# Kernel tuning notes

Hardware: AMD Instinct MI355X
Metric: run time of the kernel (lower is better)

The kernel has to match this reference:

```python
import jax, jax.numpy as jnp
import numpy as np

V = 50257   # vocab_size
D = 128     # embed_dim
B = 1024    # batch of center words
C = 10      # context window size


def setup_inputs() -> dict:
    key = jax.random.key(0)
    ks = jax.random.split(key, 12)
    s = 0.05  # small init scale for linear weights
    return {
        "center_id": jax.random.randint(ks[0], (B,), 0, V),
        "context_ids": jax.random.randint(ks[1], (B, C), 0, V),
        "epsilon": jax.random.normal(ks[2], (D,), dtype=jnp.float32),
        # embedding tables init uniform(-1, 1) as in the torch module
        "emb": jax.random.uniform(ks[3], (V, D), minval=-1.0, maxval=1.0, dtype=jnp.float32),
        "prior_means": jax.random.uniform(ks[4], (V, D), minval=-1.0, maxval=1.0, dtype=jnp.float32),
        "prior_vars": jax.random.uniform(ks[5], (V, D), minval=-1.0, maxval=1.0, dtype=jnp.float32),
        "W_enc": jax.random.normal(ks[6], (2 * D, 2 * D), dtype=jnp.float32) * s,
        "b_enc": jnp.zeros((2 * D,), dtype=jnp.float32),
        "W_mean": jax.random.normal(ks[7], (2 * D, D), dtype=jnp.float32) * s,
        "b_mean": jnp.zeros((D,), dtype=jnp.float32),
        "W_var": jax.random.normal(ks[8], (2 * D, D), dtype=jnp.float32) * s,
        "b_var": jnp.zeros((D,), dtype=jnp.float32),
        "W_vocab": jax.random.normal(ks[9], (D, V), dtype=jnp.float32) * s,
        "b_vocab": jnp.zeros((V,), dtype=jnp.float32),
    }


def reference(center_id, context_ids, epsilon, emb, prior_means, prior_vars,
              W_enc, b_enc, W_mean, b_mean, W_var, b_var, W_vocab, b_vocab):
    ce = emb[center_id]                       # [B, D]
    cx = emb[context_ids]                     # [B, C, D]
    enc_in = jnp.concatenate(
        [jnp.broadcast_to(ce[:, None, :], cx.shape), cx], axis=-1)  # [B, C, 2D]
    h = jax.nn.relu(enc_in @ W_enc + b_enc).sum(axis=1)  # [B, 2D]
    mean = h @ W_mean + b_mean                           # [B, D]
    var = jax.nn.softplus(h @ W_var + b_var)             # [B, D] (diag cov s0)
    z = mean + jnp.exp(var / 2.0) * epsilon              # single shared epsilon [D]
    logits = z @ W_vocab + b_vocab                        # [B, V]
    logp = jax.nn.log_softmax(logits, axis=1)             # log(categorical)

    pm = prior_means[center_id]                           # m1 [B, D]
    pv = jax.nn.softplus(prior_vars[center_id])           # diag cov s1 [B, D]
    diff = pm - mean
    # closed-form diagonal Gaussian KL, identical math to the
    # trace/inverse/det formulation over diagflat matrices in the source
    kl = 0.5 * jnp.sum(var / pv + diff * diff / pv - 1.0
                       + jnp.log(pv) - jnp.log(var), axis=1)  # [B]

    # reconstruction: sum_k log categorical[i, context_ids[i, k]]
    rec = jnp.take_along_axis(logp, context_ids, axis=1).sum(axis=1)  # [B]

    return jnp.mean(rec - kl)
```

## Files before the change

### kernel.cpp

```cpp
#include <hip/hip_runtime.h>
#include <math.h>

#define VV 50257
#define VPAD 50304
#define DD 128
#define BB 1024
#define CC 10

typedef short bf16x8 __attribute__((ext_vector_type(8)));
typedef float f32x4 __attribute__((ext_vector_type(4)));

__device__ inline float bf2f(unsigned short u) {
    return __uint_as_float(((unsigned)u) << 16);
}
__device__ inline unsigned short f2bf(float f) {
    unsigned u = __float_as_uint(f);
    unsigned r = ((u >> 16) & 1) + 0x7FFF;
    return (unsigned short)((u + r) >> 16);
}


__global__ __launch_bounds__(256) void k_prep(
    const float* __restrict__ Wv, const float* __restrict__ W_enc,
    unsigned short* __restrict__ WvP, unsigned short* __restrict__ WeP)
{
    const int bid = blockIdx.x, tid = threadIdx.x;

    if (bid < 786) {
        __shared__ float tile[128][65];
        const int v0 = bid * 64;
#pragma unroll
        for (int i = 0; i < 32; ++i) {
            int idx = tid + i * 256;
            int k = idx >> 6, j = idx & 63;
            int v = v0 + j;
            tile[k][j] = (v < VV) ? Wv[(size_t)k * VV + v] : 0.f;
        }
        __syncthreads();
#pragma unroll
        for (int i = 0; i < 4; ++i) {
            int c = i * 256 + tid;
            int l15 = c & 15, q = (c >> 4) & 3, kI = (c >> 6) & 3, g = c >> 8;
            bf16x8 o;
#pragma unroll
            for (int e = 0; e < 8; ++e)
                o[e] = (short)f2bf(tile[kI * 32 + q * 8 + e][g * 16 + l15]);
            size_t vg = (size_t)bid * 4 + g;
            *(bf16x8*)(WvP + ((vg * 4 + kI) * 64 + q * 16 + l15) * 8) = o;
        }
        return;
    }

    __shared__ float tl[256][17];
    const int jg = bid - 786;
#pragma unroll
    for (int i = 0; i < 16; ++i) {
        int idx = i * 256 + tid;
        int k = idx >> 4, j = idx & 15;
        tl[k][j] = W_enc[(size_t)k * 256 + jg * 16 + j];
    }
    __syncthreads();
#pragma unroll
    for (int i = 0; i < 2; ++i) {
        int c = i * 256 + tid;
        int l15 = c & 15, q = (c >> 4) & 3, kI = c >> 6;
        bf16x8 o;
#pragma unroll
        for (int e = 0; e < 8; ++e)
            o[e] = (short)f2bf(tl[kI * 32 + q * 8 + e][l15]);
        *(bf16x8*)(WeP + (((size_t)jg * 8 + kI) * 64 + q * 16 + l15) * 8) = o;
    }
}

__global__ __launch_bounds__(256) void k_enc(
    const int* __restrict__ center_id, const int* __restrict__ context_ids,
    const float* __restrict__ emb, const unsigned short* __restrict__ WeP,
    const float* __restrict__ b_enc, unsigned short* __restrict__ enc_relu)
{
    __shared__ __align__(16) unsigned short As[64 * 256];
    __shared__ __align__(16) unsigned short Cs[64][136];
    const int tid  = threadIdx.x;
    const int lane = tid & 63;
    const int wid  = tid >> 6;
    const int wm   = wid & 1;
    const int wn   = wid >> 1;
    const int quad = lane >> 4;
    const int l15  = lane & 15;

    const int b0 = blockIdx.x * 64;
    const int c  = blockIdx.y;
    const int n0 = blockIdx.z * 128;

    const int rlane = tid >> 4;
    const int c8    = tid & 15;
    const int kIc   = c8 >> 2, qc = c8 & 3;
#pragma unroll
    for (int p = 0; p < 4; ++p) {
        int r = p * 16 + rlane;
        int rid_ce = center_id[b0 + r];
        int rid_cx = context_ids[(b0 + r) * CC + c];
        const float* s0 = emb + (size_t)rid_ce * 128 + c8 * 8;
        const float* s1 = emb + (size_t)rid_cx * 128 + c8 * 8;
        float4 a0 = *(const float4*)s0, a1 = *(const float4*)(s0 + 4);
        float4 b0v = *(const float4*)s1, b1v = *(const float4*)(s1 + 4);
        bf16x8 oa, ob;
        oa[0] = (short)f2bf(a0.x); oa[1] = (short)f2bf(a0.y);
        oa[2] = (short)f2bf(a0.z); oa[3] = (short)f2bf(a0.w);
        oa[4] = (short)f2bf(a1.x); oa[5] = (short)f2bf(a1.y);
        oa[6] = (short)f2bf(a1.z); oa[7] = (short)f2bf(a1.w);
        ob[0] = (short)f2bf(b0v.x); ob[1] = (short)f2bf(b0v.y);
        ob[2] = (short)f2bf(b0v.z); ob[3] = (short)f2bf(b0v.w);
        ob[4] = (short)f2bf(b1v.x); ob[5] = (short)f2bf(b1v.y);
        ob[6] = (short)f2bf(b1v.z); ob[7] = (short)f2bf(b1v.w);
        *(bf16x8*)(As + ((p * 8 + kIc) * 64 + qc * 16 + rlane) * 8) = oa;
        *(bf16x8*)(As + ((p * 8 + kIc + 4) * 64 + qc * 16 + rlane) * 8) = ob;
    }
    __syncthreads();

    float benc[4];
#pragma unroll
    for (int nt = 0; nt < 4; ++nt)
        benc[nt] = b_enc[n0 + wn * 64 + nt * 16 + l15];

    f32x4 acc[2][4];
#pragma unroll
    for (int mt = 0; mt < 2; ++mt)
#pragma unroll
        for (int nt = 0; nt < 4; ++nt) acc[mt][nt] = (f32x4){0.f, 0.f, 0.f, 0.f};

#pragma unroll
    for (int kI = 0; kI < 8; ++kI) {
        bf16x8 a[2], b[4];
#pragma unroll
        for (int mt = 0; mt < 2; ++mt)
            a[mt] = *(const bf16x8*)(As + (((wm * 2 + mt) * 8 + kI) * 64 + lane) * 8);
#pragma unroll
        for (int nt = 0; nt < 4; ++nt) {
            size_t jg = (size_t)blockIdx.z * 8 + wn * 4 + nt;
            b[nt] = *(const bf16x8*)(WeP + ((jg * 8 + kI) * 64 + lane) * 8);
        }
#pragma unroll
        for (int mt = 0; mt < 2; ++mt)
#pragma unroll
            for (int nt = 0; nt < 4; ++nt)
                acc[mt][nt] = __builtin_amdgcn_mfma_f32_16x16x32_bf16(
                    a[mt], b[nt], acc[mt][nt], 0, 0, 0);
    }

#pragma unroll
    for (int mt = 0; mt < 2; ++mt)
#pragma unroll
        for (int nt = 0; nt < 4; ++nt) {
            int col = wn * 64 + nt * 16 + l15;
#pragma unroll
            for (int reg = 0; reg < 4; ++reg) {
                int row = wm * 32 + mt * 16 + quad * 4 + reg;
                Cs[row][col] = f2bf(fmaxf(acc[mt][nt][reg] + benc[nt], 0.f));
            }
        }
    __syncthreads();
#pragma unroll
    for (int i = 0; i < 4; ++i) {
        int ch = i * 256 + tid;
        int row = ch >> 4, cc = ch & 15;
        bf16x8 v = *(const bf16x8*)&Cs[row][cc * 8];
        *(bf16x8*)(enc_relu + ((size_t)(b0 + row) * CC + c) * 256 + n0 + cc * 8) = v;
    }
}

__global__ __launch_bounds__(128) void k_latent(
    const unsigned short* __restrict__ enc_relu, const float* __restrict__ W_mean,
    const float* __restrict__ b_mean, const float* __restrict__ W_var,
    const float* __restrict__ b_var, const float* __restrict__ epsilon,
    const int* __restrict__ center_id, const int* __restrict__ context_ids,
    const unsigned short* __restrict__ WvP, const float* __restrict__ bv,
    const float* __restrict__ prior_means, const float* __restrict__ prior_vars,
    unsigned short* __restrict__ z_pack, float* __restrict__ kl,
    float* __restrict__ ctxsum, float* __restrict__ out)
{
    __shared__ __align__(16) float hs[256];
    __shared__ float red[2];
    __shared__ float credp[CC][2];
    const int tid = threadIdx.x;
    const int b = blockIdx.x;
    const int wid = tid >> 6;

    if (b == 0 && tid == 0) out[0] = 0.f;

    {
        const int j = tid * 2;
        float s0 = 0.f, s1 = 0.f;
#pragma unroll
        for (int c = 0; c < CC; ++c) {
            ushort2 u = *(const ushort2*)(enc_relu + ((size_t)b * CC + c) * 256 + j);
            s0 += bf2f(u.x); s1 += bf2f(u.y);
        }
        hs[j] = s0; hs[j + 1] = s1;
    }
    __syncthreads();

    const int d = tid;
    float m  = b_mean[d];
    float vr = b_var[d];
    for (int k0 = 0; k0 < 256; k0 += 4) {
        float4 h4 = *(const float4*)&hs[k0];
#pragma unroll
        for (int kk = 0; kk < 4; ++kk) {
            float hk = ((const float*)&h4)[kk];
            m  += hk * W_mean[(size_t)(k0 + kk) * 128 + d];
            vr += hk * W_var[(size_t)(k0 + kk) * 128 + d];
        }
    }

    float var = (vr > 20.f) ? vr : log1pf(__expf(vr));
    float zd = m + __expf(0.5f * var) * epsilon[d];
    unsigned short zu = f2bf(zd);
    {
        const int kIz = d >> 5, qz = (d >> 3) & 3, ez = d & 7;
        const int bg = b >> 4, l15b = b & 15;
        z_pack[(((size_t)(bg * 4 + kIz)) * 64 + qz * 16 + l15b) * 8 + ez] = zu;
    }
    float zb = bf2f(zu);

    int cid = center_id[b];
    float pm  = prior_means[(size_t)cid * 128 + d];
    float pvr = prior_vars[(size_t)cid * 128 + d];
    float pv  = (pvr > 20.f) ? pvr : log1pf(__expf(pvr));
    float diff = pm - m;
    float t = var / pv + diff * diff / pv - 1.f + logf(pv) - logf(var);
#pragma unroll
    for (int off = 32; off; off >>= 1) t += __shfl_down(t, off, 64);
    if ((tid & 63) == 0) red[wid] = t;

    int cids[CC];
#pragma unroll
    for (int p = 0; p < CC; ++p) cids[p] = context_ids[b * CC + p];
    const int kIz = d >> 5, qz = (d >> 3) & 3, ez = d & 7;
    float cs[CC];
#pragma unroll
    for (int p = 0; p < CC; ++p) {
        int vg = cids[p] >> 4, l15v = cids[p] & 15;
        float w = bf2f(WvP[(((size_t)(vg * 4 + kIz)) * 64 + qz * 16 + l15v) * 8 + ez]);
        cs[p] = zb * w;
    }
#pragma unroll
    for (int p = 0; p < CC; ++p) {
#pragma unroll
        for (int off = 32; off; off >>= 1) cs[p] += __shfl_down(cs[p], off, 64);
    }
    if ((tid & 63) == 0) {
#pragma unroll
        for (int p = 0; p < CC; ++p) credp[p][wid] = cs[p];
    }
    __syncthreads();
    if (tid == 0) {
        kl[b] = 0.5f * (red[0] + red[1]);
        float c = 0.f;
#pragma unroll
        for (int p = 0; p < CC; ++p)
            c += credp[p][0] + credp[p][1] + bv[cids[p]];
        ctxsum[b] = c;
    }
}

__global__ __launch_bounds__(256) void k_lse(
    const unsigned short* __restrict__ z_pack, const unsigned short* __restrict__ WvP,
    const float* __restrict__ bv, float* __restrict__ partial)
{
    __shared__ float pl[2][128][20];
    const int tid  = threadIdx.x;
    const int lane = tid & 63;
    const int wid  = tid >> 6;
    const int wm   = wid & 1;
    const int wn   = wid >> 1;
    const int quad = lane >> 4;
    const int l15  = lane & 15;
    const int n0   = blockIdx.x * 128;
    const int mg   = blockIdx.y;

    bf16x8 bfr[4][4];
#pragma unroll
    for (int nt = 0; nt < 4; ++nt) {
        size_t vg = (size_t)blockIdx.x * 8 + wn * 4 + nt;
#pragma unroll
        for (int kI = 0; kI < 4; ++kI)
            bfr[nt][kI] = *(const bf16x8*)(WvP + ((vg * 4 + kI) * 64 + lane) * 8);
    }

    float bvf[4];
#pragma unroll
    for (int nt = 0; nt < 4; ++nt) {
        int n = n0 + wn * 64 + nt * 16 + l15;
        bvf[nt] = (n < VV) ? bv[n] : -__builtin_huge_valf();
    }

#pragma unroll
    for (int mi = 0; mi < 2; ++mi) {
        const int mi_g = mg * 2 + mi;

        f32x4 acc[4][4];
#pragma unroll
        for (int mt = 0; mt < 4; ++mt)
#pragma unroll
            for (int nt = 0; nt < 4; ++nt) acc[mt][nt] = (f32x4){0.f, 0.f, 0.f, 0.f};

#pragma unroll
        for (int kI = 0; kI < 4; ++kI) {
            bf16x8 afr[4];
#pragma unroll
            for (int mt = 0; mt < 4; ++mt) {
                size_t bg = (size_t)mi_g * 8 + wm * 4 + mt;
                afr[mt] = *(const bf16x8*)(z_pack + ((bg * 4 + kI) * 64 + lane) * 8);
            }
#pragma unroll
            for (int mt = 0; mt < 4; ++mt)
#pragma unroll
                for (int nt = 0; nt < 4; ++nt)
                    acc[mt][nt] = __builtin_amdgcn_mfma_f32_16x16x32_bf16(
                        afr[mt], bfr[nt][kI], acc[mt][nt], 0, 0, 0);
        }

#pragma unroll
        for (int mt = 0; mt < 4; ++mt)
#pragma unroll
            for (int reg = 0; reg < 4; ++reg) {
                float s = 0.f;
#pragma unroll
                for (int nt = 0; nt < 4; ++nt)
                    s += __expf(acc[mt][nt][reg] + bvf[nt]);
                pl[wn][wm * 64 + mt * 16 + quad * 4 + reg][l15] = s;
            }
        __syncthreads();
        if (tid < 128) {
            const float* p0 = &pl[0][tid][0];
            const float* p1 = &pl[1][tid][0];
            float4 a0 = *(const float4*)(p0);
            float4 a1 = *(const float4*)(p0 + 4);
            float4 a2 = *(const float4*)(p0 + 8);
            float4 a3 = *(const float4*)(p0 + 12);
            float4 b0 = *(const float4*)(p1);
            float4 b1 = *(const float4*)(p1 + 4);
            float4 b2 = *(const float4*)(p1 + 8);
            float4 b3 = *(const float4*)(p1 + 12);
            float tot = (a0.x + a0.y + a0.z + a0.w) + (a1.x + a1.y + a1.z + a1.w)
                      + (a2.x + a2.y + a2.z + a2.w) + (a3.x + a3.y + a3.z + a3.w)
                      + (b0.x + b0.y + b0.z + b0.w) + (b1.x + b1.y + b1.z + b1.w)
                      + (b2.x + b2.y + b2.z + b2.w) + (b3.x + b3.y + b3.z + b3.w);
            partial[(size_t)blockIdx.x * 1024 + mi_g * 128 + tid] = tot;
        }
        __syncthreads();
    }
}

__global__ __launch_bounds__(256) void k_reduce(
    const float* __restrict__ partial, const float* __restrict__ ctxsum,
    const float* __restrict__ kl, float* __restrict__ out)
{
    __shared__ float bred[4];
    const int tid = threadIdx.x;
    const int row = blockIdx.x * 16 + (tid >> 4);
    const int part = tid & 15;

    float s = 0.f;
    for (int vb = part; vb < 393; vb += 16)
        s += partial[(size_t)vb * 1024 + row];
    s += __shfl_xor(s, 1, 64);
    s += __shfl_xor(s, 2, 64);
    s += __shfl_xor(s, 4, 64);
    s += __shfl_xor(s, 8, 64);

    float v = 0.f;
    if (part == 0)
        v = ctxsum[row] - 10.f * logf(s) - kl[row];
    v += __shfl_xor(v, 16, 64);
    v += __shfl_xor(v, 32, 64);
    if ((tid & 63) == 0) bred[tid >> 6] = v;
    __syncthreads();
    if (tid == 0)
        atomicAdd(out, (bred[0] + bred[1] + bred[2] + bred[3]) * (1.f / 1024.f));
}

extern "C" void kernel_launch(void* const* d_in, const int* in_sizes, int n_in,
                              void* d_out, int out_size, void* d_ws, size_t ws_size,
                              hipStream_t stream)
{
    const int*   center_id   = (const int*)d_in[0];
    const int*   context_ids = (const int*)d_in[1];
    const float* epsilon     = (const float*)d_in[2];
    const float* emb         = (const float*)d_in[3];
    const float* prior_means = (const float*)d_in[4];
    const float* prior_vars  = (const float*)d_in[5];
    const float* W_enc       = (const float*)d_in[6];
    const float* b_enc       = (const float*)d_in[7];
    const float* W_mean      = (const float*)d_in[8];
    const float* b_mean      = (const float*)d_in[9];
    const float* W_var       = (const float*)d_in[10];
    const float* b_var       = (const float*)d_in[11];
    const float* W_vocab     = (const float*)d_in[12];
    const float* b_vocab     = (const float*)d_in[13];

    float* out = (float*)d_out;
    char*  ws  = (char*)d_ws;

    size_t off = 0;
    unsigned short* WvP      = (unsigned short*)(ws + off); off += 12877824;
    unsigned short* WeP      = (unsigned short*)(ws + off); off += 131072;
    unsigned short* z_pack   = (unsigned short*)(ws + off); off += 262144;
    unsigned short* enc_relu = (unsigned short*)(ws + off); off += 5242880;
    float*          kl       = (float*)(ws + off);          off += 4096;
    float*          ctxsum   = (float*)(ws + off);          off += 4096;
    float*          partial  = (float*)(ws + off);          off += 1609728;

    k_prep<<<802, 256, 0, stream>>>(W_vocab, W_enc, WvP, WeP);
    k_enc<<<dim3(16, 10, 2), 256, 0, stream>>>(center_id, context_ids, emb, WeP,
                                               b_enc, enc_relu);
    k_latent<<<1024, 128, 0, stream>>>(enc_relu, W_mean, b_mean, W_var, b_var,
                                       epsilon, center_id, context_ids, WvP,
                                       b_vocab, prior_means, prior_vars,
                                       z_pack, kl, ctxsum, out);
    k_lse<<<dim3(393, 4), 256, 0, stream>>>(z_pack, WvP, b_vocab, partial);
    k_reduce<<<64, 256, 0, stream>>>(partial, ctxsum, kl, out);
}
```

Measured before the change: 215.1 us.

## Fuse final reduction into LSE kernel, pack mean/var weights as bf16, pad LDS

```diff
diff --git a/kernel.cpp b/kernel.cpp
--- a/kernel.cpp
+++ b/kernel.cpp
@@ -6,6 +6,7 @@
 #define DD 128
 #define BB 1024
 #define CC 10
+#define NLSE 1572
 
 typedef short bf16x8 __attribute__((ext_vector_type(8)));
 typedef float f32x4 __attribute__((ext_vector_type(4)));
@@ -22,7 +23,9 @@
 
 __global__ __launch_bounds__(256) void k_prep(
     const float* __restrict__ Wv, const float* __restrict__ W_enc,
-    unsigned short* __restrict__ WvP, unsigned short* __restrict__ WeP)
+    const float* __restrict__ W_mean, const float* __restrict__ W_var,
+    unsigned short* __restrict__ WvP, unsigned short* __restrict__ WeP,
+    unsigned short* __restrict__ Wmv)
 {
     const int bid = blockIdx.x, tid = threadIdx.x;
 
@@ -51,33 +54,46 @@
         return;
     }
 
-    __shared__ float tl[256][17];
-    const int jg = bid - 786;
-#pragma unroll
-    for (int i = 0; i < 16; ++i) {
-        int idx = i * 256 + tid;
-        int k = idx >> 4, j = idx & 15;
-        tl[k][j] = W_enc[(size_t)k * 256 + jg * 16 + j];
-    }
-    __syncthreads();
-#pragma unroll
-    for (int i = 0; i < 2; ++i) {
-        int c = i * 256 + tid;
-        int l15 = c & 15, q = (c >> 4) & 3, kI = c >> 6;
-        bf16x8 o;
-#pragma unroll
-        for (int e = 0; e < 8; ++e)
-            o[e] = (short)f2bf(tl[kI * 32 + q * 8 + e][l15]);
-        *(bf16x8*)(WeP + (((size_t)jg * 8 + kI) * 64 + q * 16 + l15) * 8) = o;
-    }
-}
-
+    if (bid < 802) {
+        __shared__ float tl[256][17];
+        const int jg = bid - 786;
+#pragma unroll
+        for (int i = 0; i < 16; ++i) {
+            int idx = i * 256 + tid;
+            int k = idx >> 4, j = idx & 15;
+            tl[k][j] = W_enc[(size_t)k * 256 + jg * 16 + j];
+        }
+        __syncthreads();
+#pragma unroll
+        for (int i = 0; i < 2; ++i) {
+            int c = i * 256 + tid;
+            int l15 = c & 15, q = (c >> 4) & 3, kI = c >> 6;
+            bf16x8 o;
+#pragma unroll
+            for (int e = 0; e < 8; ++e)
+                o[e] = (short)f2bf(tl[kI * 32 + q * 8 + e][l15]);
+            *(bf16x8*)(WeP + (((size_t)jg * 8 + kI) * 64 + q * 16 + l15) * 8) = o;
+        }
+        return;
+    }
+
+    const int b4 = bid - 802;
+#pragma unroll
+    for (int i = 0; i < 32; ++i) {
+        int idx = b4 * 8192 + i * 256 + tid;
+        unsigned short m = f2bf(W_mean[idx]);
+        unsigned short v = f2bf(W_var[idx]);
+        *(ushort2*)(Wmv + (size_t)idx * 2) = make_ushort2(m, v);
+    }
+}
+
+#define AS_STRIDE 520
 __global__ __launch_bounds__(256) void k_enc(
     const int* __restrict__ center_id, const int* __restrict__ context_ids,
     const float* __restrict__ emb, const unsigned short* __restrict__ WeP,
     const float* __restrict__ b_enc, unsigned short* __restrict__ enc_relu)
 {
-    __shared__ __align__(16) unsigned short As[64 * 256];
+    __shared__ __align__(16) unsigned short As[32 * AS_STRIDE];
     __shared__ __align__(16) unsigned short Cs[64][136];
     const int tid  = threadIdx.x;
     const int lane = tid & 63;
@@ -112,8 +128,8 @@
         ob[2] = (short)f2bf(b0v.z); ob[3] = (short)f2bf(b0v.w);
         ob[4] = (short)f2bf(b1v.x); ob[5] = (short)f2bf(b1v.y);
         ob[6] = (short)f2bf(b1v.z); ob[7] = (short)f2bf(b1v.w);
-        *(bf16x8*)(As + ((p * 8 + kIc) * 64 + qc * 16 + rlane) * 8) = oa;
-        *(bf16x8*)(As + ((p * 8 + kIc + 4) * 64 + qc * 16 + rlane) * 8) = ob;
+        *(bf16x8*)(As + (size_t)(p * 8 + kIc) * AS_STRIDE + (qc * 16 + rlane) * 8) = oa;
+        *(bf16x8*)(As + (size_t)(p * 8 + kIc + 4) * AS_STRIDE + (qc * 16 + rlane) * 8) = ob;
     }
     __syncthreads();
 
@@ -133,7 +149,7 @@
         bf16x8 a[2], b[4];
 #pragma unroll
         for (int mt = 0; mt < 2; ++mt)
-            a[mt] = *(const bf16x8*)(As + (((wm * 2 + mt) * 8 + kI) * 64 + lane) * 8);
+            a[mt] = *(const bf16x8*)(As + (size_t)((wm * 2 + mt) * 8 + kI) * AS_STRIDE + lane * 8);
 #pragma unroll
         for (int nt = 0; nt < 4; ++nt) {
             size_t jg = (size_t)blockIdx.z * 8 + wn * 4 + nt;
@@ -169,14 +185,14 @@
 }
 
 __global__ __launch_bounds__(128) void k_latent(
-    const unsigned short* __restrict__ enc_relu, const float* __restrict__ W_mean,
-    const float* __restrict__ b_mean, const float* __restrict__ W_var,
-    const float* __restrict__ b_var, const float* __restrict__ epsilon,
+    const unsigned short* __restrict__ enc_relu, const unsigned short* __restrict__ Wmv,
+    const float* __restrict__ b_mean, const float* __restrict__ b_var,
+    const float* __restrict__ epsilon,
     const int* __restrict__ center_id, const int* __restrict__ context_ids,
     const unsigned short* __restrict__ WvP, const float* __restrict__ bv,
     const float* __restrict__ prior_means, const float* __restrict__ prior_vars,
-    unsigned short* __restrict__ z_pack, float* __restrict__ kl,
-    float* __restrict__ ctxsum, float* __restrict__ out)
+    unsigned short* __restrict__ z_pack, float* __restrict__ base,
+    float* __restrict__ sumexp, int* __restrict__ counter)
 {
     __shared__ __align__(16) float hs[256];
     __shared__ float red[2];
@@ -185,7 +201,10 @@
     const int b = blockIdx.x;
     const int wid = tid >> 6;
 
-    if (b == 0 && tid == 0) out[0] = 0.f;
+    if (tid == 0) {
+        sumexp[b] = 0.f;
+        if (b == 0) *counter = 0;
+    }
 
     {
         const int j = tid * 2;
@@ -207,16 +226,17 @@
 #pragma unroll
         for (int kk = 0; kk < 4; ++kk) {
             float hk = ((const float*)&h4)[kk];
-            m  += hk * W_mean[(size_t)(k0 + kk) * 128 + d];
-            vr += hk * W_var[(size_t)(k0 + kk) * 128 + d];
+            ushort2 u = *(const ushort2*)(Wmv + ((size_t)(k0 + kk) * 128 + d) * 2);
+            m  += hk * bf2f(u.x);
+            vr += hk * bf2f(u.y);
         }
     }
 
     float var = (vr > 20.f) ? vr : log1pf(__expf(vr));
     float zd = m + __expf(0.5f * var) * epsilon[d];
     unsigned short zu = f2bf(zd);
+    const int kIz = d >> 5, qz = (d >> 3) & 3, ez = d & 7;
     {
-        const int kIz = d >> 5, qz = (d >> 3) & 3, ez = d & 7;
         const int bg = b >> 4, l15b = b & 15;
         z_pack[(((size_t)(bg * 4 + kIz)) * 64 + qz * 16 + l15b) * 8 + ez] = zu;
     }
@@ -235,7 +255,6 @@
     int cids[CC];
 #pragma unroll
     for (int p = 0; p < CC; ++p) cids[p] = context_ids[b * CC + p];
-    const int kIz = d >> 5, qz = (d >> 3) & 3, ez = d & 7;
     float cs[CC];
 #pragma unroll
     for (int p = 0; p < CC; ++p) {
@@ -254,20 +273,24 @@
     }
     __syncthreads();
     if (tid == 0) {
-        kl[b] = 0.5f * (red[0] + red[1]);
+        float klv = 0.5f * (red[0] + red[1]);
         float c = 0.f;
 #pragma unroll
         for (int p = 0; p < CC; ++p)
             c += credp[p][0] + credp[p][1] + bv[cids[p]];
-        ctxsum[b] = c;
+        base[b] = c - klv;
     }
 }
 
 __global__ __launch_bounds__(256) void k_lse(
     const unsigned short* __restrict__ z_pack, const unsigned short* __restrict__ WvP,
-    const float* __restrict__ bv, float* __restrict__ partial)
+    const float* __restrict__ bv, const float* __restrict__ base,
+    float* __restrict__ sumexp, int* __restrict__ counter,
+    float* __restrict__ out)
 {
     __shared__ float pl[2][128][20];
+    __shared__ float fred[4];
+    __shared__ int isLast;
     const int tid  = threadIdx.x;
     const int lane = tid & 63;
     const int wid  = tid >> 6;
@@ -346,38 +369,30 @@
                       + (a2.x + a2.y + a2.z + a2.w) + (a3.x + a3.y + a3.z + a3.w)
                       + (b0.x + b0.y + b0.z + b0.w) + (b1.x + b1.y + b1.z + b1.w)
                       + (b2.x + b2.y + b2.z + b2.w) + (b3.x + b3.y + b3.z + b3.w);
-            partial[(size_t)blockIdx.x * 1024 + mi_g * 128 + tid] = tot;
+            atomicAdd(&sumexp[mi_g * 128 + tid], tot);
         }
         __syncthreads();
     }
-}
-
-__global__ __launch_bounds__(256) void k_reduce(
-    const float* __restrict__ partial, const float* __restrict__ ctxsum,
-    const float* __restrict__ kl, float* __restrict__ out)
-{
-    __shared__ float bred[4];
-    const int tid = threadIdx.x;
-    const int row = blockIdx.x * 16 + (tid >> 4);
-    const int part = tid & 15;
-
+
+    __threadfence();
+    if (tid == 0) {
+        int prev = atomicAdd(counter, 1);
+        isLast = (prev == NLSE - 1);
+    }
+    __syncthreads();
+    if (!isLast) return;
+    __threadfence();
+
+    const volatile float* sv = sumexp;
     float s = 0.f;
-    for (int vb = part; vb < 393; vb += 16)
-        s += partial[(size_t)vb * 1024 + row];
-    s += __shfl_xor(s, 1, 64);
-    s += __shfl_xor(s, 2, 64);
-    s += __shfl_xor(s, 4, 64);
-    s += __shfl_xor(s, 8, 64);
-
-    float v = 0.f;
-    if (part == 0)
-        v = ctxsum[row] - 10.f * logf(s) - kl[row];
-    v += __shfl_xor(v, 16, 64);
-    v += __shfl_xor(v, 32, 64);
-    if ((tid & 63) == 0) bred[tid >> 6] = v;
+    for (int i = tid; i < 1024; i += 256)
+        s += base[i] - 10.f * logf(sv[i]);
+#pragma unroll
+    for (int off = 32; off; off >>= 1) s += __shfl_down(s, off, 64);
+    if ((tid & 63) == 0) fred[tid >> 6] = s;
     __syncthreads();
     if (tid == 0)
-        atomicAdd(out, (bred[0] + bred[1] + bred[2] + bred[3]) * (1.f / 1024.f));
+        out[0] = (fred[0] + fred[1] + fred[2] + fred[3]) * (1.f / 1024.f);
 }
 
 extern "C" void kernel_launch(void* const* d_in, const int* in_sizes, int n_in,
@@ -405,19 +420,20 @@
     size_t off = 0;
     unsigned short* WvP      = (unsigned short*)(ws + off); off += 12877824;
     unsigned short* WeP      = (unsigned short*)(ws + off); off += 131072;
+    unsigned short* Wmv      = (unsigned short*)(ws + off); off += 131072;
     unsigned short* z_pack   = (unsigned short*)(ws + off); off += 262144;
     unsigned short* enc_relu = (unsigned short*)(ws + off); off += 5242880;
-    float*          kl       = (float*)(ws + off);          off += 4096;
-    float*          ctxsum   = (float*)(ws + off);          off += 4096;
-    float*          partial  = (float*)(ws + off);          off += 1609728;
-
-    k_prep<<<802, 256, 0, stream>>>(W_vocab, W_enc, WvP, WeP);
+    float*          base     = (float*)(ws + off);          off += 4096;
+    float*          sumexp   = (float*)(ws + off);          off += 4096;
+    int*            counter  = (int*)(ws + off);            off += 64;
+
+    k_prep<<<806, 256, 0, stream>>>(W_vocab, W_enc, W_mean, W_var, WvP, WeP, Wmv);
     k_enc<<<dim3(16, 10, 2), 256, 0, stream>>>(center_id, context_ids, emb, WeP,
                                                b_enc, enc_relu);
-    k_latent<<<1024, 128, 0, stream>>>(enc_relu, W_mean, b_mean, W_var, b_var,
-                                       epsilon, center_id, context_ids, WvP,
-                                       b_vocab, prior_means, prior_vars,
-                                       z_pack, kl, ctxsum, out);
-    k_lse<<<dim3(393, 4), 256, 0, stream>>>(z_pack, WvP, b_vocab, partial);
-    k_reduce<<<64, 256, 0, stream>>>(partial, ctxsum, kl, out);
-}
+    k_latent<<<1024, 128, 0, stream>>>(enc_relu, Wmv, b_mean, b_var, epsilon,
+                                       center_id, context_ids, WvP, b_vocab,
+                                       prior_means, prior_vars, z_pack, base,
+                                       sumexp, counter);
+    k_lse<<<dim3(393, 4), 256, 0, stream>>>(z_pack, WvP, b_vocab, base,
+                                            sumexp, counter, out);
+}
```

New measurement: 303.8 us. 41.3% more time.
